# Performance work log

Measured on AMD Instinct MI355X. Metric: run time of the kernel, lower is better.

Reference implementation:

```python
import jax, jax.numpy as jnp
import numpy as np

SR = 16000
N_FFT = 1024
HOP = 256
WIN = 1024
N_MELS = 80
EPS = 1e-8
DRY_W, RIR_W = 3.0, 1.0
TIME_W, FREQ_W, MEL_W = 1.0, 0.5, 0.3
CONSIST_W, RIR_REG_W = 0.2, 0.1


def _hann(n):
    # torch.hann_window(periodic=True)
    return (0.5 - 0.5 * jnp.cos(2.0 * jnp.pi * jnp.arange(n) / n)).astype(jnp.float32)


def _stft(x):
    """torchaudio.transforms.Spectrogram(power=None, normalized=True) equivalent.
    x: [..., T] -> complex [..., n_freqs, n_frames]"""
    shp = x.shape
    T = shp[-1]
    xf = x.reshape(-1, T)
    pad = N_FFT // 2
    xp = jnp.pad(xf, ((0, 0), (pad, pad)), mode='reflect')  # center=True
    n_frames = 1 + T // HOP
    idx = jnp.arange(n_frames)[:, None] * HOP + jnp.arange(N_FFT)[None, :]
    win = _hann(WIN)
    frames = xp[:, idx] * win[None, None, :]              # [N, frames, n_fft]
    spec = jnp.fft.rfft(frames, axis=-1)                  # [N, frames, freqs]
    spec = spec / jnp.sqrt(jnp.sum(win ** 2))             # normalized='window'
    return spec.reshape(shp[:-1] + (n_frames, N_FFT // 2 + 1)).swapaxes(-1, -2)


def _mel_fb():
    # torchaudio melscale_fbanks, htk scale, norm=None, f_min=0, f_max=sr/2
    n_freqs = N_FFT // 2 + 1
    all_freqs = np.linspace(0.0, SR / 2.0, n_freqs)
    hz2mel = lambda f: 2595.0 * np.log10(1.0 + f / 700.0)
    mel2hz = lambda m: 700.0 * (10.0 ** (m / 2595.0) - 1.0)
    m_pts = np.linspace(hz2mel(0.0), hz2mel(SR / 2.0), N_MELS + 2)
    f_pts = mel2hz(m_pts)
    f_diff = f_pts[1:] - f_pts[:-1]
    slopes = f_pts[None, :] - all_freqs[:, None]
    down = -slopes[:, :-2] / f_diff[:-1]
    up = slopes[:, 2:] / f_diff[1:]
    fb = np.maximum(0.0, np.minimum(down, up))
    return jnp.asarray(fb, jnp.float32)  # [n_freqs, n_mels]

_FB = _mel_fb()


def _l1(a, b):
    return jnp.mean(jnp.abs(a - b))


def _freq_loss(pred, target):
    ps, ts = _stft(pred), _stft(target)
    mag_loss = _l1(jnp.abs(ps), jnp.abs(ts))
    dphi = jnp.angle(ps) - jnp.angle(ts)
    # cosine sim of unit [cos, sin] vectors == cos(delta phase)
    phase_loss = 1.0 - jnp.mean(jnp.cos(dphi))
    return mag_loss + 0.1 * phase_loss


def _mel_loss(pred, target):
    pm = jnp.einsum('...ft,fm->...mt', jnp.abs(_stft(pred)) ** 2, _FB)
    tm = jnp.einsum('...ft,fm->...mt', jnp.abs(_stft(target)) ** 2, _FB)
    return _l1(jnp.log(pm + EPS), jnp.log(tm + EPS))


def _consistency_loss(pred_dry, pred_rir, mix):
    # full linear convolution along time, truncated to first T samples
    T = pred_dry.shape[-1]
    n = 2 * T
    D = jnp.fft.rfft(pred_dry, n=n, axis=-1)
    R = jnp.fft.rfft(pred_rir, n=n, axis=-1)
    rec = jnp.fft.irfft(D * R, n=n, axis=-1)[..., :T]
    return _l1(rec, mix[..., :T])


def _rir_reg_loss(pred_rir):
    T = pred_rir.shape[-1]
    sparsity = jnp.mean(jnp.abs(pred_rir))
    seg = T // 4
    decay = 0.0
    for i in range(3):
        e1 = jnp.mean(pred_rir[:, :, i * seg:(i + 1) * seg] ** 2)
        e2 = jnp.mean(pred_rir[:, :, (i + 1) * seg:(i + 2) * seg] ** 2)
        decay = decay + jax.nn.relu(e2 - 0.8 * e1)
    return sparsity + decay


def setup_inputs() -> dict:
    key = jax.random.key(0)
    ks = jax.random.split(key, 5)
    shape = (32, 2, 64000)
    names = ['pred_dry', 'pred_rir', 'target_dry', 'target_rir', 'mix']
    return {n: jax.random.normal(k, shape, dtype=jnp.float32) for n, k in zip(names, ks)}


def reference(pred_dry, pred_rir, target_dry, target_rir, mix):
    dry_time = _l1(pred_dry, target_dry)
    dry_freq = _freq_loss(pred_dry, target_dry)
    dry_mel = _mel_loss(pred_dry, target_dry)
    total_dry = TIME_W * dry_time + FREQ_W * dry_freq + MEL_W * dry_mel

    rir_time = _l1(pred_rir, target_rir)
    rir_reg = _rir_reg_loss(pred_rir)
    total_rir = rir_time + RIR_REG_W * rir_reg

    consist = _consistency_loss(pred_dry, pred_rir, mix)
    total = DRY_W * total_dry + RIR_W * total_rir + CONSIST_W * consist
    return total
```

## Files before the change

kernel.cpp:

```cpp
#include <hip/hip_runtime.h>
#include <math.h>

#define ROWS 64
#define TLEN 64000
#define NFR 251
#define NMELS 80
#define NFB 131072
#define PI2F 6.28318530717958647692f
#define PI_F 3.14159265358979323846f

__device__ double g_part[64][12];

__device__ constexpr int DR[16] = {0,4,8,12,1,5,9,13,2,6,10,14,3,7,11,15};
__device__ constexpr int RM[16] = {0,3,2,1,15,14,13,12,11,10,9,8,7,6,5,4};

__device__ inline int dr4(int i){ return ((i & 3) << 2) | (i >> 2); }
__device__ inline int SW(int k){ return k + (k >> 5); }

__device__ inline void atomAddD(double* p, double v){
  __hip_atomic_fetch_add(p, v, __ATOMIC_RELAXED, __HIP_MEMORY_SCOPE_AGENT);
}
__device__ inline int brev6(int x){ return (int)((unsigned)__brev((unsigned)x) >> 26); }
__device__ inline float2 cmul(float2 a, float2 b){
  return make_float2(a.x*b.x - a.y*b.y, a.x*b.y + a.y*b.x);
}
__device__ inline float wred(float v){
#pragma unroll
  for (int o = 32; o > 0; o >>= 1) v += __shfl_down(v, o, 64);
  return v;
}

template<int S, int N>
__device__ inline void fft64_lanes(float2* v, int l){
  float2 W[5];
#pragma unroll
  for (int si = 0; si < 5; ++si){
    int d = 32 >> si;
    float a = (float)S * PI_F * (float)(l & (d-1)) * (1.0f/(float)d);
    float sn, cs; __sincosf(a, &sn, &cs);
    W[si] = make_float2(cs, sn);
  }
#pragma unroll
  for (int si = 0; si < 6; ++si){
    int d = 32 >> si;
    bool hi = (l & d) != 0;
#pragma unroll
    for (int rr = 0; rr < N; ++rr){
      float2 x = v[rr];
      float tx = __shfl_xor(x.x, d, 64);
      float ty = __shfl_xor(x.y, d, 64);
      float sx = x.x + tx, sy = x.y + ty;
      float dx = tx - x.x, dy = ty - x.y;
      float rx, ry;
      if (si < 5){ rx = dx*W[si].x - dy*W[si].y; ry = dx*W[si].y + dy*W[si].x; }
      else       { rx = dx; ry = dy; }
      v[rr].x = hi ? rx : sx;
      v[rr].y = hi ? ry : sy;
    }
  }
}

template<int S>
__device__ inline void fft16_reg(float2* v){
  const float Sf = (float)S;
  const float C1 = 0.9238795325112867f, S1 = 0.3826834323650898f, C2 = 0.7071067811865476f;
  const float2 W1[4] = {{1.f,0.f},{C1,Sf*S1},{C2,Sf*C2},{S1,Sf*C1}};
  const float2 W2[4] = {{1.f,0.f},{C2,Sf*C2},{0.f,Sf},{-C2,Sf*C2}};
  const float2 W3[4] = {{1.f,0.f},{S1,Sf*C1},{-C2,Sf*C2},{-C1,-Sf*S1}};
#pragma unroll
  for (int j = 0; j < 4; ++j){
    float2 x0=v[j], x1=v[j+4], x2=v[j+8], x3=v[j+12];
    float2 t0={x0.x+x2.x, x0.y+x2.y}, t1={x0.x-x2.x, x0.y-x2.y};
    float2 t2={x1.x+x3.x, x1.y+x3.y}, t3={x1.x-x3.x, x1.y-x3.y};
    float2 y0={t0.x+t2.x, t0.y+t2.y};
    float2 y2={t0.x-t2.x, t0.y-t2.y};
    float2 y1={t1.x - Sf*t3.y, t1.y + Sf*t3.x};
    float2 y3={t1.x + Sf*t3.y, t1.y - Sf*t3.x};
    v[j]=y0; v[j+4]=cmul(y1,W1[j]); v[j+8]=cmul(y2,W2[j]); v[j+12]=cmul(y3,W3[j]);
  }
#pragma unroll
  for (int b = 0; b < 4; ++b){
    float2 x0=v[4*b], x1=v[4*b+1], x2=v[4*b+2], x3=v[4*b+3];
    float2 t0={x0.x+x2.x, x0.y+x2.y}, t1={x0.x-x2.x, x0.y-x2.y};
    float2 t2={x1.x+x3.x, x1.y+x3.y}, t3={x1.x-x3.x, x1.y-x3.y};
    v[4*b]   = make_float2(t0.x+t2.x, t0.y+t2.y);
    v[4*b+2] = make_float2(t0.x-t2.x, t0.y-t2.y);
    v[4*b+1] = make_float2(t1.x - Sf*t3.y, t1.y + Sf*t3.x);
    v[4*b+3] = make_float2(t1.x + Sf*t3.y, t1.y - Sf*t3.x);
  }
}

template<int S>
__device__ inline void fft1024_wave(float2* v, int l){
  fft16_reg<S>(v);
  float a = (float)S * PI2F * (float)l * (1.0f/1024.0f);
  float sn, cs; __sincosf(a, &sn, &cs);
  float2 T = make_float2(cs, sn);
  float2 cur = T;
#pragma unroll
  for (int k2 = 1; k2 < 16; ++k2){
    v[DR[k2]] = cmul(v[DR[k2]], cur);
    if (k2 < 15) cur = cmul(cur, T);
  }
  fft64_lanes<S,16>(v, l);
}

template<int S>
__device__ inline void fft128_wave(float2* v, int l){
  float2 a = {v[0].x+v[1].x, v[0].y+v[1].y};
  float2 b = {v[0].x-v[1].x, v[0].y-v[1].y};
  float ang = (float)S * PI_F * (float)l * (1.0f/64.0f);
  float sn, cs; __sincosf(ang, &sn, &cs);
  v[0] = a; v[1] = cmul(b, make_float2(cs, sn));
  fft64_lanes<S,2>(v, l);
}

template<int N>
__device__ inline void ifft64_lanes(float2* v, int l){
  float2 W[5];
#pragma unroll
  for (int si = 0; si < 5; ++si){
    int d = 32 >> si;
    float a = PI_F * (float)(l & (d-1)) * (1.0f/(float)d);
    float sn, cs; __sincosf(a, &sn, &cs);
    W[si] = make_float2(cs, sn);
  }
#pragma unroll
  for (int si = 5; si >= 0; --si){
    int d = 32 >> si;
    bool hi = (l & d) != 0;
#pragma unroll
    for (int rr = 0; rr < N; ++rr){
      float2 x = v[rr];
      float2 xp = x;
      if (si < 5 && hi) xp = cmul(x, W[si]);
      float tx = __shfl_xor(xp.x, d, 64);
      float ty = __shfl_xor(xp.y, d, 64);
      v[rr].x = hi ? (tx - xp.x) : (xp.x + tx);
      v[rr].y = hi ? (ty - xp.y) : (xp.y + ty);
    }
  }
}

__device__ inline void r4p(float2* v, int i0, int i1, int i2, int i3){
  float2 x0=v[i0], x1=v[i1], x2=v[i2], x3=v[i3];
  float2 t0={x0.x+x2.x, x0.y+x2.y}, t1={x0.x-x2.x, x0.y-x2.y};
  float2 t2={x1.x+x3.x, x1.y+x3.y}, t3={x1.x-x3.x, x1.y-x3.y};
  v[i0] = make_float2(t0.x+t2.x, t0.y+t2.y);
  v[i2] = make_float2(t0.x-t2.x, t0.y-t2.y);
  v[i1] = make_float2(t1.x - t3.y, t1.y + t3.x);
  v[i3] = make_float2(t1.x + t3.y, t1.y - t3.x);
}

__device__ inline void ifft16_reg(float2* v){
#pragma unroll
  for (int b = 0; b < 4; ++b) r4p(v, 4*b, 4*b+1, 4*b+2, 4*b+3);
  const float C1 = 0.9238795325112867f, S1 = 0.3826834323650898f, C2 = 0.7071067811865476f;
  const float2 W1[4] = {{1.f,0.f},{C1,S1},{C2,C2},{S1,C1}};
  const float2 W2[4] = {{1.f,0.f},{C2,C2},{0.f,1.f},{-C2,C2}};
  const float2 W3[4] = {{1.f,0.f},{S1,C1},{-C2,C2},{-C1,-S1}};
#pragma unroll
  for (int j = 1; j < 4; ++j){
    v[j+4]  = cmul(v[j+4],  W1[j]);
    v[j+8]  = cmul(v[j+8],  W2[j]);
    v[j+12] = cmul(v[j+12], W3[j]);
  }
#pragma unroll
  for (int j = 0; j < 4; ++j) r4p(v, j, j+4, j+8, j+12);
}

__device__ inline void ifft128_wave(float2* v, int l){
  ifft64_lanes<2>(v, l);
  float ang = PI_F * (float)l * (1.0f/64.0f);
  float sn, cs; __sincosf(ang, &sn, &cs);
  v[1] = cmul(v[1], make_float2(cs, sn));
  float2 a = {v[0].x+v[1].x, v[0].y+v[1].y};
  float2 b = {v[0].x-v[1].x, v[0].y-v[1].y};
  v[0] = a; v[1] = b;
}

__device__ inline void ifft1024_wave(float2* v, int l){
  ifft64_lanes<16>(v, l);
  float a = PI2F * (float)l * (1.0f/1024.0f);
  float sn, cs; __sincosf(a, &sn, &cs);
  float2 T = make_float2(cs, sn);
  float2 cur = T;
#pragma unroll
  for (int k2 = 1; k2 < 16; ++k2){
    v[DR[k2]] = cmul(v[DR[k2]], cur);
    if (k2 < 15) cur = cmul(cur, T);
  }
  ifft16_reg(v);
}

extern "C" __global__ void __launch_bounds__(256) k_init(){
  int t = blockIdx.x*256 + threadIdx.x;
  if (t < 768) ((double*)g_part)[t] = 0.0;
}

extern "C" __global__ void __launch_bounds__(256) k_time(
    const float* __restrict__ pd, const float* __restrict__ td,
    const float* __restrict__ pr, const float* __restrict__ tr){
  const int N4 = ROWS*TLEN/4;
  int stride = gridDim.x * 256;
  float sdt=0.f, srt=0.f, ssp=0.f, e0=0.f, e1=0.f, e2=0.f, e3=0.f;
  const float4* pd4 = (const float4*)pd;
  const float4* td4 = (const float4*)td;
  const float4* pr4 = (const float4*)pr;
  const float4* tr4 = (const float4*)tr;
  for (int i = blockIdx.x*256 + threadIdx.x; i < N4; i += stride){
    float4 a = pd4[i], b = td4[i], p = pr4[i], q = tr4[i];
    sdt += fabsf(a.x-b.x)+fabsf(a.y-b.y)+fabsf(a.z-b.z)+fabsf(a.w-b.w);
    srt += fabsf(p.x-q.x)+fabsf(p.y-q.y)+fabsf(p.z-q.z)+fabsf(p.w-q.w);
    ssp += fabsf(p.x)+fabsf(p.y)+fabsf(p.z)+fabsf(p.w);
    float p2 = p.x*p.x + p.y*p.y + p.z*p.z + p.w*p.w;
    int seg = (i % 16000) / 4000;
    if (seg == 0) e0 += p2; else if (seg == 1) e1 += p2;
    else if (seg == 2) e2 += p2; else e3 += p2;
  }
  sdt = wred(sdt); srt = wred(srt); ssp = wred(ssp);
  e0 = wred(e0); e1 = wred(e1); e2 = wred(e2); e3 = wred(e3);
  if ((threadIdx.x & 63) == 0){
    int bank = (blockIdx.x*4 + (threadIdx.x >> 6)) & 63;
    atomAddD(&g_part[bank][0], (double)sdt);
    atomAddD(&g_part[bank][1], (double)srt);
    atomAddD(&g_part[bank][2], (double)ssp);
    atomAddD(&g_part[bank][3], (double)e0);
    atomAddD(&g_part[bank][4], (double)e1);
    atomAddD(&g_part[bank][5], (double)e2);
    atomAddD(&g_part[bank][6], (double)e3);
  }
}

extern "C" __global__ void __launch_bounds__(64) k_stft(
    const float* __restrict__ pd, const float* __restrict__ td){
  __shared__ float2 spec0[64];
  __shared__ float2 pt[530];
  int l = threadIdx.x;
  int frame = (blockIdx.x & 7) * (ROWS*NFR/8) + (blockIdx.x >> 3);
  int r = frame / NFR, fr = frame - r*NFR;
  const float* pdr = pd + (size_t)r*TLEN;
  const float* tdr = td + (size_t)r*TLEN;
  const float scale = 0.05103103630798288f;
  int base = fr*256 - 512;
  float2 v[16];
#pragma unroll
  for (int m = 0; m < 16; ++m){
    int j = l + 64*m;
    int g = base + j;
    g = (g < 0) ? -g : ((g >= TLEN) ? (2*TLEN - 2 - g) : g);
    float w = (0.5f - 0.5f*__cosf((PI2F/1024.0f)*(float)j)) * scale;
    v[m] = make_float2(pdr[g]*w, tdr[g]*w);
  }
  fft1024_wave<-1>(v, l);
  int kb = brev6(l);
  spec0[kb] = v[0];
  float magp = 0.f, cosp = 0.f;
#pragma unroll
  for (int rr = 1; rr < 16; ++rr){
    float2 z = v[rr];
    float2 zm;
    zm.x = __shfl_xor(v[RM[rr]].x, 63, 64);
    zm.y = __shfl_xor(v[RM[rr]].y, 63, 64);
    int k = DR[rr] + 16*kb;
    float px = 0.5f*(z.x + zm.x), py = 0.5f*(z.y - zm.y);
    float tx = 0.5f*(z.y + zm.y), ty = -0.5f*(z.x - zm.x);
    float ppk = px*px + py*py, ttk = tx*tx + ty*ty;
    float rp = rsqrtf(fmaxf(ppk, 1e-30f)), rt = rsqrtf(fmaxf(ttk, 1e-30f));
    magp += 0.5f*fabsf(ppk*rp - ttk*rt);
    cosp += 0.5f*((px*tx + py*ty)*rp*rt);
    int kk = (k <= 512) ? k : 1024 - k;
    pt[SW(kk)] = make_float2(ppk, ttk);
  }
  if (l <= 32){
    float2 z  = spec0[l];
    float2 zm = spec0[(64 - l) & 63];
    float px = 0.5f*(z.x + zm.x), py = 0.5f*(z.y - zm.y);
    float tx = 0.5f*(z.y + zm.y), ty = -0.5f*(z.x - zm.x);
    float ppk = px*px + py*py, ttk = tx*tx + ty*ty;
    float rp = rsqrtf(fmaxf(ppk, 1e-30f)), rt = rsqrtf(fmaxf(ttk, 1e-30f));
    magp += fabsf(ppk*rp - ttk*rt);
    cosp += (px*tx + py*ty)*rp*rt;
    pt[SW(16*l)] = make_float2(ppk, ttk);
  }
  float melp = 0.f;
  const float C = (2595.0f * log10f(1.0f + 8000.0f/700.0f))
                  * (1.0f/81.0f) * (1.0f/2595.0f) * 2.302585093f;
  const float df = 15.625f;
  {
    int m = l;
    float f0 = 700.0f*(__expf(C*(float)(m  )) - 1.0f);
    float f1 = 700.0f*(__expf(C*(float)(m+1)) - 1.0f);
    float f2 = 700.0f*(__expf(C*(float)(m+2)) - 1.0f);
    float i1 = 1.0f/(f1 - f0), i2 = 1.0f/(f2 - f1);
    int lo = (int)ceilf(f0 * (1.0f/df));  if (lo < 0) lo = 0;
    int hi = (int)floorf(f2 * (1.0f/df)); if (hi > 512) hi = 512;
    float pm = 0.f, tm = 0.f;
#pragma unroll 2
    for (int k = lo; k <= hi; ++k){
      float frq = df*(float)k;
      float c = fmaxf(fminf((frq - f0)*i1, (f2 - frq)*i2), 0.f);
      float2 w = pt[SW(k)];
      pm += c*w.x; tm += c*w.y;
    }
    melp += fabsf(__logf(pm + 1e-8f) - __logf(tm + 1e-8f));
  }
  {
    int m = 64 + (l >> 2), q = l & 3;
    float f0 = 700.0f*(__expf(C*(float)(m  )) - 1.0f);
    float f1 = 700.0f*(__expf(C*(float)(m+1)) - 1.0f);
    float f2 = 700.0f*(__expf(C*(float)(m+2)) - 1.0f);
    float i1 = 1.0f/(f1 - f0), i2 = 1.0f/(f2 - f1);
    int lo = (int)ceilf(f0 * (1.0f/df));  if (lo < 0) lo = 0;
    int hi = (int)floorf(f2 * (1.0f/df)); if (hi > 512) hi = 512;
    int n = hi - lo + 1;
    int ch = (n + 3) >> 2;
    int k0 = lo + q*ch;
    int k1 = k0 + ch; if (k1 > hi + 1) k1 = hi + 1;
    float pm = 0.f, tm = 0.f;
#pragma unroll 2
    for (int k = k0; k < k1; ++k){
      float frq = df*(float)k;
      float c = fmaxf(fminf((frq - f0)*i1, (f2 - frq)*i2), 0.f);
      float2 w = pt[SW(k)];
      pm += c*w.x; tm += c*w.y;
    }
    pm += __shfl_xor(pm, 1, 64); pm += __shfl_xor(pm, 2, 64);
    tm += __shfl_xor(tm, 1, 64); tm += __shfl_xor(tm, 2, 64);
    if (q == 0)
      melp += fabsf(__logf(pm + 1e-8f) - __logf(tm + 1e-8f));
  }
  magp = wred(magp); cosp = wred(cosp); melp = wred(melp);
  if (l == 0){
    int bank = blockIdx.x & 63;
    atomAddD(&g_part[bank][7], (double)magp);
    atomAddD(&g_part[bank][8], (double)cosp);
    atomAddD(&g_part[bank][9], (double)melp);
  }
}

extern "C" __global__ void __launch_bounds__(512) k_fwd1(
    const float* __restrict__ pd, const float* __restrict__ pr,
    float2* __restrict__ buf, int row0){
  __shared__ float SM[10256];
  float* LA = SM;
  float* LB = SM + 5000;
  float2* LT = (float2*)SM;
  int wid = threadIdx.x >> 6, l = threadIdx.x & 63;
  int tid = threadIdx.x;
  int rl = blockIdx.y;
  int n1base = blockIdx.x * 8;
  int n1 = n1base + wid;
  const float* a = pd + (size_t)(row0+rl)*TLEN;
  const float* b = pr + (size_t)(row0+rl)*TLEN;
  for (int i = tid; i < 2000; i += 512){
    int n2 = i >> 2, wp = (i & 3)*2;
    float2 va = *(const float2*)&a[n1base + wp + 128*n2];
    float2 vb = *(const float2*)&b[n1base + wp + 128*n2];
    *(float2*)&LA[n2*10 + wp] = va;
    *(float2*)&LB[n2*10 + wp] = vb;
  }
  __syncthreads();
  float2 v[16];
#pragma unroll
  for (int m = 0; m < 16; ++m){
    int n2 = l + 64*m;
    if (n2 < 500) v[m] = make_float2(LA[n2*10 + wid], LB[n2*10 + wid]);
    else          v[m] = make_float2(0.f, 0.f);
  }
  __syncthreads();
  fft1024_wave<-1>(v, l);
  int kb = brev6(l);
  const float tw = -(PI2F / (float)NFB);
#pragma unroll
  for (int rr = 0; rr < 16; ++rr){
    int K = DR[rr] + 16*kb;
    float ang = tw * (float)(n1*K);
    float sn, cs; __sincosf(ang, &sn, &cs);
    v[rr] = cmul(v[rr], make_float2(cs, sn));
  }
  float2* rowp = buf + (size_t)rl*NFB;
#pragma unroll
  for (int c = 0; c < 2; ++c){
#pragma unroll
    for (int rrl = 0; rrl < 8; ++rrl)
      LT[wid*513 + rrl*64 + l] = v[c*8 + rrl];
    __syncthreads();
#pragma unroll
    for (int it = 0; it < 4; ++it){
      int g = (tid + it*512)*2;
      int s = g >> 3, nw = g & 7;
      float2 x = LT[nw*513 + s], y = LT[(nw+1)*513 + s];
      *(float4*)&rowp[(size_t)(c*512 + s)*128 + n1base + nw] =
          make_float4(x.x, x.y, y.x, y.y);
    }
    __syncthreads();
  }
}

__device__ inline float2 pointmul(float2 z, float2 zm){
  float Dx = 0.5f*(z.x + zm.x), Dy = 0.5f*(z.y - zm.y);
  float Rx = 0.5f*(z.y + zm.y), Ry = -0.5f*(z.x - zm.x);
  return make_float2(Dx*Rx - Dy*Ry, Dx*Ry + Dy*Rx);
}

extern "C" __global__ void __launch_bounds__(256) k_mid(float2* __restrict__ buf){
  int wid = threadIdx.x >> 6, l = threadIdx.x & 63;
  int p = blockIdx.x*4 + wid;
  if (p > 512) return;
  int k2A = p, k2B = (1024 - p) & 1023;
  int sA = dr4(k2A & 15)*64 + brev6(k2A >> 4);
  int sB = dr4(k2B & 15)*64 + brev6(k2B >> 4);
  float2* base = buf + (size_t)blockIdx.y*NFB;
  float2* rA = base + (size_t)sA*128;
  float2* rB = base + (size_t)sB*128;
  bool pair = (sB != sA);
  float2 vA[2] = { rA[l], rA[l+64] };
  float2 vB[2];
  if (pair){ vB[0] = rB[l]; vB[1] = rB[l+64]; }
  fft128_wave<-1>(vA, l);
  if (pair) fft128_wave<-1>(vB, l);
  float2 cA[2];
  if (p == 0){
    int kb = brev6(l);
    int q0 = brev6((64 - kb) & 63);
    float2 zm0 = { __shfl(vA[0].x, q0, 64), __shfl(vA[0].y, q0, 64) };
    float2 zm1 = { __shfl_xor(vA[1].x, 63, 64), __shfl_xor(vA[1].y, 63, 64) };
    cA[0] = pointmul(vA[0], zm0);
    cA[1] = pointmul(vA[1], zm1);
  } else {
    const float2* src = pair ? vB : vA;
    float2 zm0 = { __shfl_xor(src[1].x, 63, 64), __shfl_xor(src[1].y, 63, 64) };
    float2 zm1 = { __shfl_xor(src[0].x, 63, 64), __shfl_xor(src[0].y, 63, 64) };
    cA[0] = pointmul(vA[0], zm0);
    cA[1] = pointmul(vA[1], zm1);
  }
  float2 cB[2];
  if (pair){
    cB[0] = make_float2( __shfl_xor(cA[1].x, 63, 64), -__shfl_xor(cA[1].y, 63, 64) );
    cB[1] = make_float2( __shfl_xor(cA[0].x, 63, 64), -__shfl_xor(cA[0].y, 63, 64) );
  }
  const float twi = PI2F / (float)NFB;
  ifft128_wave(cA, l);
#pragma unroll
  for (int rr = 0; rr < 2; ++rr){
    int n1 = l + 64*rr;
    float ang = twi * (float)(n1*k2A);
    float sn, cs; __sincosf(ang, &sn, &cs);
    rA[n1] = cmul(cA[rr], make_float2(cs, sn));
  }
  if (pair){
    ifft128_wave(cB, l);
#pragma unroll
    for (int rr = 0; rr < 2; ++rr){
      int n1 = l + 64*rr;
      float ang = twi * (float)(n1*k2B);
      float sn, cs; __sincosf(ang, &sn, &cs);
      rB[n1] = cmul(cB[rr], make_float2(cs, sn));
    }
  }
}

extern "C" __global__ void __launch_bounds__(512) k_inv2(
    const float* __restrict__ mix, float2* __restrict__ buf, int row0){
  __shared__ float SM[10256];
  float2* LT = (float2*)SM;
  float* LM = SM;
  int wid = threadIdx.x >> 6, l = threadIdx.x & 63;
  int tid = threadIdx.x;
  int rl = blockIdx.y;
  int n1base = blockIdx.x * 8;
  float2* rowp = buf + (size_t)rl*NFB;
  float2 v[16];
#pragma unroll
  for (int c = 0; c < 2; ++c){
#pragma unroll
    for (int it = 0; it < 4; ++it){
      int g = (tid + it*512)*2;
      int s = g >> 3, nw = g & 7;
      float4 q = *(const float4*)&rowp[(size_t)(c*512 + s)*128 + n1base + nw];
      LT[nw*513 + s]     = make_float2(q.x, q.y);
      LT[(nw+1)*513 + s] = make_float2(q.z, q.w);
    }
    __syncthreads();
#pragma unroll
    for (int rrl = 0; rrl < 8; ++rrl)
      v[c*8 + rrl] = LT[wid*513 + rrl*64 + l];
    __syncthreads();
  }
  const float* mr = mix + (size_t)(row0+rl)*TLEN;
  for (int i = tid; i < 2000; i += 512){
    int n2 = i >> 2, wp = (i & 3)*2;
    *(float2*)&LM[n2*10 + wp] = *(const float2*)&mr[n1base + wp + 128*n2];
  }
  ifft1024_wave(v, l);
  __syncthreads();
  const float invn = 1.0f/(float)NFB;
  float acc = 0.f;
#pragma unroll
  for (int m = 0; m < 16; ++m){
    int n2 = l + 64*m;
    if (n2 < 500)
      acc += fabsf(v[m].x*invn - LM[n2*10 + wid]);
  }
  acc = wred(acc);
  if (l == 0){
    int bank = (blockIdx.x*8 + wid + blockIdx.y*16) & 63;
    atomAddD(&g_part[bank][10], (double)acc);
  }
}

extern "C" __global__ void __launch_bounds__(64) k_finalize(float* __restrict__ out){
  __shared__ double s[12];
  int t = threadIdx.x;
  if (t < 12){
    double v = 0.0;
    for (int b = 0; b < 64; ++b) v += g_part[b][t];
    s[t] = v;
  }
  __syncthreads();
  if (t == 0){
    double dt = s[0] / 4096000.0;
    double rt = s[1] / 4096000.0;
    double sp = s[2] / 4096000.0;
    double e0 = s[3] / 1024000.0, e1 = s[4] / 1024000.0;
    double e2 = s[5] / 1024000.0, e3 = s[6] / 1024000.0;
    double dec = fmax(e1 - 0.8*e0, 0.0) + fmax(e2 - 0.8*e1, 0.0) + fmax(e3 - 0.8*e2, 0.0);
    double c1 = 8240832.0;
    double freq = s[7]/c1 + 0.1*(1.0 - s[8]/c1);
    double mel  = s[9] / 1285120.0;
    double cons = s[10] / 4096000.0;
    double total = 3.0*(dt + 0.5*freq + 0.3*mel)
                 + (rt + 0.1*(sp + dec))
                 + 0.2*cons;
    out[0] = (float)total;
  }
}

extern "C" void kernel_launch(void* const* d_in, const int* in_sizes, int n_in,
                              void* d_out, int out_size, void* d_ws, size_t ws_size,
                              hipStream_t stream){
  const float* pd = (const float*)d_in[0];
  const float* pr = (const float*)d_in[1];
  const float* td = (const float*)d_in[2];
  const float* tr = (const float*)d_in[3];
  const float* mx = (const float*)d_in[4];
  float* out = (float*)d_out;
  float2* buf = (float2*)d_ws;

  size_t rowBytes = (size_t)NFB * sizeof(float2);
  int maxrows = (int)(ws_size / rowBytes);
  if (maxrows > ROWS) maxrows = ROWS;
  if (maxrows < 1) maxrows = 1;
  int nch = (ROWS + maxrows - 1) / maxrows;
  int chrows = (ROWS + nch - 1) / nch;

  hipLaunchKernelGGL(k_init, dim3(3), dim3(256), 0, stream);
  hipLaunchKernelGGL(k_time, dim3(2048), dim3(256), 0, stream, pd, td, pr, tr);
  hipLaunchKernelGGL(k_stft, dim3(ROWS*NFR), dim3(64), 0, stream, pd, td);
  for (int row0 = 0; row0 < ROWS; row0 += chrows){
    int nr = ROWS - row0; if (nr > chrows) nr = chrows;
    hipLaunchKernelGGL(k_fwd1, dim3(16, nr),  dim3(512), 0, stream, pd, pr, buf, row0);
    hipLaunchKernelGGL(k_mid,  dim3(129, nr), dim3(256), 0, stream, buf);
    hipLaunchKernelGGL(k_inv2, dim3(16, nr),  dim3(512), 0, stream, mx, buf, row0);
  }
  hipLaunchKernelGGL(k_finalize, dim3(1), dim3(64), 0, stream, out);
}
```

Baseline: 311.3 us.

## Replace lane-shuffle radix-2 FFT64 stage with LDS-based radix-8x8 transform

Inside the STFT kernel, the cross-lane 64-point FFT, previously done as six radix-2 shuffle stages, is replaced by two radix-8 passes that exchange data through a 512-entry shared-memory scratch buffer with XOR swizzling. The output is now in natural lane order, so the bit-reversal index is dropped. The aim is fewer shuffle instructions and fewer twiddle computations. In exchange it adds several __syncthreads barriers and LDS traffic per 8-element half, which can cost more than the shuffles it removes.

```diff
diff --git a/kernel.cpp b/kernel.cpp
--- a/kernel.cpp
+++ b/kernel.cpp
@@ -113,6 +113,96 @@
   float sn, cs; __sincosf(ang, &sn, &cs);
   v[0] = a; v[1] = cmul(b, make_float2(cs, sn));
   fft64_lanes<S,2>(v, l);
+}
+
+template<int S>
+__device__ inline void fft8p(float2* y){
+  const float Sf = (float)S;
+  const float C2 = 0.7071067811865476f;
+  float2 t0={y[0].x+y[4].x, y[0].y+y[4].y};
+  float2 t1={y[1].x+y[5].x, y[1].y+y[5].y};
+  float2 t2={y[2].x+y[6].x, y[2].y+y[6].y};
+  float2 t3={y[3].x+y[7].x, y[3].y+y[7].y};
+  float2 u0={y[0].x-y[4].x, y[0].y-y[4].y};
+  float2 u1={y[1].x-y[5].x, y[1].y-y[5].y};
+  float2 u2={y[2].x-y[6].x, y[2].y-y[6].y};
+  float2 u3={y[3].x-y[7].x, y[3].y-y[7].y};
+  { float x=u1.x, yy=u1.y; u1.x = C2*(x - Sf*yy); u1.y = C2*(Sf*x + yy); }
+  { float x=u2.x, yy=u2.y; u2.x = -Sf*yy;         u2.y = Sf*x; }
+  { float x=u3.x, yy=u3.y; u3.x = -C2*(x + Sf*yy); u3.y = C2*(Sf*x - yy); }
+  {
+    float2 e0={t0.x+t2.x,t0.y+t2.y}, e1={t0.x-t2.x,t0.y-t2.y};
+    float2 o0={t1.x+t3.x,t1.y+t3.y}, o1={t1.x-t3.x,t1.y-t3.y};
+    y[0]=make_float2(e0.x+o0.x, e0.y+o0.y);
+    y[4]=make_float2(e0.x-o0.x, e0.y-o0.y);
+    y[2]=make_float2(e1.x - Sf*o1.y, e1.y + Sf*o1.x);
+    y[6]=make_float2(e1.x + Sf*o1.y, e1.y - Sf*o1.x);
+  }
+  {
+    float2 e0={u0.x+u2.x,u0.y+u2.y}, e1={u0.x-u2.x,u0.y-u2.y};
+    float2 o0={u1.x+u3.x,u1.y+u3.y}, o1={u1.x-u3.x,u1.y-u3.y};
+    y[1]=make_float2(e0.x+o0.x, e0.y+o0.y);
+    y[5]=make_float2(e0.x-o0.x, e0.y-o0.y);
+    y[3]=make_float2(e1.x - Sf*o1.y, e1.y + Sf*o1.x);
+    y[7]=make_float2(e1.x + Sf*o1.y, e1.y - Sf*o1.x);
+  }
+}
+
+template<int S>
+__device__ inline void fft64_lds(float2* v, int l, float2* scr){
+  int s = l >> 3, a = l & 7;
+  int sw = (s & 1);
+#pragma unroll
+  for (int h = 0; h < 2; ++h){
+    float2* vh = v + 8*h;
+#pragma unroll
+    for (int r = 0; r < 8; ++r) scr[r*64 + l] = vh[r];
+    __syncthreads();
+    float2 y[8];
+#pragma unroll
+    for (int j = 0; j < 8; ++j)
+      y[j] = scr[s*64 + a + 8*((j + s) & 7)];
+    fft8p<S>(y);
+    {
+      float ang = (float)S * PI2F * (float)l * (1.0f/64.0f);
+      float sn, cs; __sincosf(ang, &sn, &cs);
+      float2 b1 = make_float2(cs, sn), cur = b1;
+#pragma unroll
+      for (int c = 1; c < 8; ++c){
+        y[c] = cmul(y[c], cur);
+        if (c < 7) cur = cmul(cur, b1);
+      }
+    }
+    __syncthreads();
+#pragma unroll
+    for (int c = 0; c < 8; ++c)
+      scr[s*64 + a + 8*(c ^ sw)] = y[c];
+    __syncthreads();
+    float2 z[8];
+#pragma unroll
+    for (int j = 0; j < 8; ++j)
+      z[j] = scr[s*64 + ((j + s) & 7) + 8*(a ^ sw)];
+    fft8p<S>(z);
+    {
+      float ang2 = (float)S * PI2F * (float)s * 0.125f;
+      float sn2, cs2; __sincosf(ang2, &sn2, &cs2);
+      float2 b2 = make_float2(cs2, sn2), cur = b2;
+#pragma unroll
+      for (int d = 1; d < 8; ++d){
+        z[d] = cmul(z[d], cur);
+        if (d < 7) cur = cmul(cur, b2);
+      }
+    }
+    __syncthreads();
+#pragma unroll
+    for (int d = 0; d < 8; ++d)
+      scr[s*64 + a + 8*(d ^ sw)] = z[d];
+    __syncthreads();
+#pragma unroll
+    for (int r = 0; r < 8; ++r)
+      vh[r] = scr[r*64 + (l ^ ((r & 1) << 3))];
+    __syncthreads();
+  }
 }
 
 template<int N>
@@ -234,6 +324,7 @@
 
 extern "C" __global__ void __launch_bounds__(64) k_stft(
     const float* __restrict__ pd, const float* __restrict__ td){
+  __shared__ float2 scr[512];
   __shared__ float2 spec0[64];
   __shared__ float2 pt[530];
   int l = threadIdx.x;
@@ -252,9 +343,20 @@
     float w = (0.5f - 0.5f*__cosf((PI2F/1024.0f)*(float)j)) * scale;
     v[m] = make_float2(pdr[g]*w, tdr[g]*w);
   }
-  fft1024_wave<-1>(v, l);
-  int kb = brev6(l);
-  spec0[kb] = v[0];
+  fft16_reg<-1>(v);
+  {
+    float a = -PI2F * (float)l * (1.0f/1024.0f);
+    float sn, cs; __sincosf(a, &sn, &cs);
+    float2 T = make_float2(cs, sn);
+    float2 cur = T;
+#pragma unroll
+    for (int k2 = 1; k2 < 16; ++k2){
+      v[DR[k2]] = cmul(v[DR[k2]], cur);
+      if (k2 < 15) cur = cmul(cur, T);
+    }
+  }
+  fft64_lds<-1>(v, l, scr);
+  spec0[l] = v[0];
   float magp = 0.f, cosp = 0.f;
 #pragma unroll
   for (int rr = 1; rr < 16; ++rr){
@@ -262,7 +364,7 @@
     float2 zm;
     zm.x = __shfl_xor(v[RM[rr]].x, 63, 64);
     zm.y = __shfl_xor(v[RM[rr]].y, 63, 64);
-    int k = DR[rr] + 16*kb;
+    int k = DR[rr] + 16*l;
     float px = 0.5f*(z.x + zm.x), py = 0.5f*(z.y - zm.y);
     float tx = 0.5f*(z.y + zm.y), ty = -0.5f*(z.x - zm.x);
     float ppk = px*px + py*py, ttk = tx*tx + ty*ty;
```

After: 296.8 us. 1.05x faster.
